# Kernel tuning notes

Measured on AMD Instinct MI355X. Metric: run time of the kernel, lower is better.

## Reference

```python
import jax, jax.numpy as jnp
import numpy as np
import math

B, T, D, H, FF = 2, 2048, 1024, 16, 4096
DH = D // H
EPS = 1e-5

def _ternary(key, out_f, in_f):
    # TFLELayer: ternary-quantized linear weight in {-1,0,1} (stored as f32 here)
    return jax.random.randint(key, (out_f, in_f), -1, 2).astype(jnp.float32)

def setup_inputs() -> dict:
    key = jax.random.key(0)
    ks = jax.random.split(key, 8)
    x = jax.random.normal(ks[0], (B, T, D), dtype=jnp.float32)
    mask = jnp.triu(jnp.ones((T, T), dtype=bool), k=1)  # True = masked (causal)
    return {
        "x": x,
        "mask": mask,
        "ln1_g": jnp.ones((D,), jnp.float32), "ln1_b": jnp.zeros((D,), jnp.float32),
        "ln2_g": jnp.ones((D,), jnp.float32), "ln2_b": jnp.zeros((D,), jnp.float32),
        "Wq": _ternary(ks[1], D, D), "Wk": _ternary(ks[2], D, D),
        "Wv": _ternary(ks[3], D, D), "Wo": _ternary(ks[4], D, D),
        "Wff1": _ternary(ks[5], FF, D), "Wff2": _ternary(ks[6], D, FF),
    }

def _ln(x, g, b):
    mu = jnp.mean(x, axis=-1, keepdims=True)
    var = jnp.var(x, axis=-1, keepdims=True)
    return (x - mu) * jax.lax.rsqrt(var + EPS) * g + b

def reference(x, mask, ln1_g, ln1_b, ln2_g, ln2_b, Wq, Wk, Wv, Wo, Wff1, Wff2):
    h = _ln(x, ln1_g, ln1_b)
    q = (h @ Wq.T).reshape(B, T, H, DH).transpose(0, 2, 1, 3)  # (B,H,T,DH)
    k = (h @ Wk.T).reshape(B, T, H, DH).transpose(0, 2, 1, 3)
    v = (h @ Wv.T).reshape(B, T, H, DH).transpose(0, 2, 1, 3)
    scale = 1.0 / math.sqrt(DH)
    attn = jnp.einsum('bhqd,bhkd->bhqk', q, k) * scale
    attn = jnp.where(mask[None, None], -jnp.inf, attn)
    attn = jax.nn.softmax(attn, axis=-1)
    out = jnp.einsum('bhqk,bhkd->bhqd', attn, v)
    out = out.transpose(0, 2, 1, 3).reshape(B, T, D) @ Wo.T
    x = x + out
    h = _ln(x, ln2_g, ln2_b)
    ff = jax.nn.gelu(h @ Wff1.T, approximate=False)
    ff = ff @ Wff2.T
    return x + ff
```

## Files before the change

### kernel.cpp

```cpp
#include <hip/hip_runtime.h>

typedef __bf16 bf16;
typedef bf16 bf16x8 __attribute__((ext_vector_type(8)));
typedef bf16 bf16x4 __attribute__((ext_vector_type(4)));
typedef float f32x4 __attribute__((ext_vector_type(4)));

static __device__ __forceinline__ void async16(const void* g, void* l) {
  __builtin_amdgcn_global_load_lds((__attribute__((address_space(1))) void*)g,
                                   (__attribute__((address_space(3))) void*)l,
                                   16, 0, 0);
}

template <int N>
static __device__ __forceinline__ float ror16(float x) {
  const int y =
      __builtin_amdgcn_update_dpp(0, __float_as_int(x), 0x120 | N, 0xf, 0xf, true);
  return __int_as_float(y);
}
static __device__ __forceinline__ float rowmax16(float x) {
  x = fmaxf(x, ror16<8>(x));
  x = fmaxf(x, ror16<4>(x));
  x = fmaxf(x, ror16<2>(x));
  x = fmaxf(x, ror16<1>(x));
  return x;
}
static __device__ __forceinline__ float rowsum16(float x) {
  x += ror16<8>(x);
  x += ror16<4>(x);
  x += ror16<2>(x);
  x += ror16<1>(x);
  return x;
}

__global__ __launch_bounds__(256) void ln1_cvt4(
    const float* __restrict__ x, const float* __restrict__ g,
    const float* __restrict__ b, bf16* __restrict__ hi, bf16* __restrict__ lo,
    const float* __restrict__ Wq, const float* __restrict__ Wk,
    const float* __restrict__ Wv, const float* __restrict__ Wo,
    bf16* __restrict__ wdst) {
  const int tid = threadIdx.x;
  if (blockIdx.x >= 4096) {
    const size_t i = ((size_t)(blockIdx.x - 4096) * 256 + tid) * 4;
    const size_t M1 = 1u << 20;
    const float* src = (i < M1) ? Wq : (i < 2 * M1) ? Wk : (i < 3 * M1) ? Wv : Wo;
    const size_t off = i & (M1 - 1);
    const float4 v = *(const float4*)(src + off);
    bf16x4 o = {(bf16)v.x, (bf16)v.y, (bf16)v.z, (bf16)v.w};
    *(bf16x4*)(wdst + i) = o;
    return;
  }
  const int row = blockIdx.x;
  const float* xr = x + (size_t)row * 1024;
  float v[4];
  float s1 = 0.f, s2 = 0.f;
#pragma unroll
  for (int j = 0; j < 4; ++j) {
    v[j] = xr[j * 256 + tid];
    s1 += v[j];
    s2 += v[j] * v[j];
  }
#pragma unroll
  for (int off = 1; off < 64; off <<= 1) {
    s1 += __shfl_xor(s1, off);
    s2 += __shfl_xor(s2, off);
  }
  __shared__ float ws1[4], ws2[4];
  const int wid = tid >> 6;
  if ((tid & 63) == 0) {
    ws1[wid] = s1;
    ws2[wid] = s2;
  }
  __syncthreads();
  s1 = ws1[0] + ws1[1] + ws1[2] + ws1[3];
  s2 = ws2[0] + ws2[1] + ws2[2] + ws2[3];
  const float mu = s1 * (1.f / 1024.f);
  const float var = s2 * (1.f / 1024.f) - mu * mu;
  const float rstd = 1.0f / sqrtf(var + 1e-5f);
#pragma unroll
  for (int j = 0; j < 4; ++j) {
    const int cc = j * 256 + tid;
    const float y = (v[j] - mu) * rstd * g[cc] + b[cc];
    const bf16 yh = (bf16)y;
    hi[(size_t)row * 1024 + cc] = yh;
    lo[(size_t)row * 1024 + cc] = (bf16)(y - (float)yh);
  }
}

__global__ __launch_bounds__(256) void ln_kernel(
    const float* __restrict__ x, const float* __restrict__ g,
    const float* __restrict__ b, bf16* __restrict__ hi) {
  const int row = blockIdx.x;
  const int tid = threadIdx.x;
  const float* xr = x + (size_t)row * 1024;
  float v[4];
  float s1 = 0.f, s2 = 0.f;
#pragma unroll
  for (int j = 0; j < 4; ++j) {
    v[j] = xr[j * 256 + tid];
    s1 += v[j];
    s2 += v[j] * v[j];
  }
#pragma unroll
  for (int off = 1; off < 64; off <<= 1) {
    s1 += __shfl_xor(s1, off);
    s2 += __shfl_xor(s2, off);
  }
  __shared__ float ws1[4], ws2[4];
  const int wid = tid >> 6;
  if ((tid & 63) == 0) {
    ws1[wid] = s1;
    ws2[wid] = s2;
  }
  __syncthreads();
  s1 = ws1[0] + ws1[1] + ws1[2] + ws1[3];
  s2 = ws2[0] + ws2[1] + ws2[2] + ws2[3];
  const float mu = s1 * (1.f / 1024.f);
  const float var = s2 * (1.f / 1024.f) - mu * mu;
  const float rstd = 1.0f / sqrtf(var + 1e-5f);
#pragma unroll
  for (int j = 0; j < 4; ++j) {
    const int cc = j * 256 + tid;
    const float y = (v[j] - mu) * rstd * g[cc] + b[cc];
    hi[(size_t)row * 1024 + cc] = (bf16)y;
  }
}

template <int EPI, bool SPLIT>
static __device__ __forceinline__ void gemm_body(
    const bf16* __restrict__ A, const bf16* __restrict__ A2,
    const bf16* __restrict__ B, void* __restrict__ Cv,
    const float* __restrict__ R, bf16* smem, int col0, int row0, int M, int N,
    int K) {
  bf16* sA = smem;
  bf16* sB = smem + 4096;
  const int tid = threadIdx.x;
  const int lane = tid & 63;
  const int wid = tid >> 6;
  const int wm = wid >> 1, wn = wid & 1;

  f32x4 acc[4][4];
  const f32x4 fzero = {0.f, 0.f, 0.f, 0.f};
#pragma unroll
  for (int i = 0; i < 4; ++i)
#pragma unroll
    for (int j = 0; j < 4; ++j) acc[i][j] = fzero;

  const int nk = K >> 5;
  const int total = SPLIT ? (nk << 1) : nk;
  const int r0 = tid >> 2, c0 = (tid & 3) << 3;
  const int r1 = (256 + tid) >> 2, c1 = ((256 + tid) & 3) << 3;
  bf16* lA0 = sA + (wid << 6) * 8;
  bf16* lA1 = sA + (256 + (wid << 6)) * 8;
  bf16* lB0 = sB + (wid << 6) * 8;
  bf16* lB1 = sB + (256 + (wid << 6)) * 8;

  for (int kt = 0; kt < total; ++kt) {
    const int kk = (kt < nk) ? kt : kt - nk;
    const bf16* Ap = (SPLIT && kt >= nk) ? A2 : A;
    const int k0 = kk << 5;
    async16(Ap + (size_t)(row0 + r0) * K + k0 + c0, lA0);
    async16(Ap + (size_t)(row0 + r1) * K + k0 + c1, lA1);
    async16(B + (size_t)(col0 + r0) * K + k0 + c0, lB0);
    async16(B + (size_t)(col0 + r1) * K + k0 + c1, lB1);
    __syncthreads();
    const int fr = lane & 15, fq = (lane >> 4) << 3;
    bf16x8 af[4], bfr[4];
#pragma unroll
    for (int i = 0; i < 4; ++i)
      af[i] = *(const bf16x8*)&sA[(wm * 64 + i * 16 + fr) * 32 + fq];
#pragma unroll
    for (int j = 0; j < 4; ++j)
      bfr[j] = *(const bf16x8*)&sB[(wn * 64 + j * 16 + fr) * 32 + fq];
#pragma unroll
    for (int i = 0; i < 4; ++i)
#pragma unroll
      for (int j = 0; j < 4; ++j)
        acc[i][j] = __builtin_amdgcn_mfma_f32_16x16x32_bf16(af[i], bfr[j],
                                                            acc[i][j], 0, 0, 0);
    __syncthreads();
  }

  const int fr = lane & 15, fq4 = (lane >> 4) << 2;
#pragma unroll
  for (int i = 0; i < 4; ++i) {
#pragma unroll
    for (int j = 0; j < 4; ++j) {
      const int rbase = row0 + wm * 64 + i * 16 + fq4;
      const int col = col0 + wn * 64 + j * 16 + fr;
      if constexpr (EPI == 5) {
        const int b = rbase >> 11, t = rbase & 2047;
        const int hh = col >> 6, d = col & 63;
        bf16x4 o4 = {(bf16)acc[i][j][0], (bf16)acc[i][j][1],
                     (bf16)acc[i][j][2], (bf16)acc[i][j][3]};
        *(bf16x4*)&((bf16*)Cv)[(((size_t)(b * 16 + hh)) * 64 + d) * 2048 + t] =
            o4;
      } else {
#pragma unroll
        for (int r = 0; r < 4; ++r) {
          const size_t idx = (size_t)(rbase + r) * N + col;
          const float val = acc[i][j][r];
          if constexpr (EPI == 0) {
            ((float*)Cv)[idx] = val;
          } else if constexpr (EPI == 2) {
            ((float*)Cv)[idx] = val + R[idx];
          } else {
            ((bf16*)Cv)[idx] =
                (bf16)(0.5f * val * (1.0f + erff(val * 0.7071067811865476f)));
          }
        }
      }
    }
  }
}

template <int EPI, bool SPLIT>
__global__ __launch_bounds__(256) void gemm_bt(
    const bf16* __restrict__ A, const bf16* __restrict__ A2,
    const bf16* __restrict__ B, void* __restrict__ Cv,
    const float* __restrict__ R, int M, int N, int K) {
  __shared__ bf16 smem[8192];
  gemm_body<EPI, SPLIT>(A, A2, B, Cv, R, smem, blockIdx.x * 128,
                        blockIdx.y * 128, M, N, K);
}

static __device__ __forceinline__ void gemm_split_merged(
    const bf16* __restrict__ A, const bf16* __restrict__ A2,
    const bf16* __restrict__ B, bf16* __restrict__ Chi, bf16* __restrict__ Clo,
    bf16* smem, float scale, int col0, int row0) {
  constexpr int K = 1024, N = 1024;
  bf16* sAh = smem;
  bf16* sAl = smem + 4096;
  bf16* sB = smem + 8192;
  const int tid = threadIdx.x;
  const int lane = tid & 63;
  const int wid = tid >> 6;
  const int wm = wid >> 1, wn = wid & 1;

  f32x4 acc[4][4];
  const f32x4 fzero = {0.f, 0.f, 0.f, 0.f};
#pragma unroll
  for (int i = 0; i < 4; ++i)
#pragma unroll
    for (int j = 0; j < 4; ++j) acc[i][j] = fzero;

  const int r0 = tid >> 2, c0 = (tid & 3) << 3;
  const int r1 = (256 + tid) >> 2, c1 = ((256 + tid) & 3) << 3;
  bf16* lAh0 = sAh + (wid << 6) * 8;
  bf16* lAh1 = sAh + (256 + (wid << 6)) * 8;
  bf16* lAl0 = sAl + (wid << 6) * 8;
  bf16* lAl1 = sAl + (256 + (wid << 6)) * 8;
  bf16* lB0 = sB + (wid << 6) * 8;
  bf16* lB1 = sB + (256 + (wid << 6)) * 8;

  for (int kt = 0; kt < 32; ++kt) {
    const int k0 = kt << 5;
    async16(A + (size_t)(row0 + r0) * K + k0 + c0, lAh0);
    async16(A + (size_t)(row0 + r1) * K + k0 + c1, lAh1);
    async16(A2 + (size_t)(row0 + r0) * K + k0 + c0, lAl0);
    async16(A2 + (size_t)(row0 + r1) * K + k0 + c1, lAl1);
    async16(B + (size_t)(col0 + r0) * K + k0 + c0, lB0);
    async16(B + (size_t)(col0 + r1) * K + k0 + c1, lB1);
    __syncthreads();
    const int fr = lane & 15, fq = (lane >> 4) << 3;
    bf16x8 ah[4], al[4], bfr[4];
#pragma unroll
    for (int i = 0; i < 4; ++i) {
      ah[i] = *(const bf16x8*)&sAh[(wm * 64 + i * 16 + fr) * 32 + fq];
      al[i] = *(const bf16x8*)&sAl[(wm * 64 + i * 16 + fr) * 32 + fq];
    }
#pragma unroll
    for (int j = 0; j < 4; ++j)
      bfr[j] = *(const bf16x8*)&sB[(wn * 64 + j * 16 + fr) * 32 + fq];
#pragma unroll
    for (int i = 0; i < 4; ++i)
#pragma unroll
      for (int j = 0; j < 4; ++j) {
        acc[i][j] = __builtin_amdgcn_mfma_f32_16x16x32_bf16(ah[i], bfr[j],
                                                            acc[i][j], 0, 0, 0);
        acc[i][j] = __builtin_amdgcn_mfma_f32_16x16x32_bf16(al[i], bfr[j],
                                                            acc[i][j], 0, 0, 0);
      }
    __syncthreads();
  }

  const int fr = lane & 15, fq4 = (lane >> 4) << 2;
#pragma unroll
  for (int i = 0; i < 4; ++i)
#pragma unroll
    for (int j = 0; j < 4; ++j) {
      const int rbase = row0 + wm * 64 + i * 16 + fq4;
      const int col = col0 + wn * 64 + j * 16 + fr;
#pragma unroll
      for (int r = 0; r < 4; ++r) {
        const size_t idx = (size_t)(rbase + r) * N + col;
        const float vs = acc[i][j][r] * scale;
        const bf16 hi = (bf16)vs;
        Chi[idx] = hi;
        Clo[idx] = (bf16)(vs - (float)hi);
      }
    }
}

__global__ __launch_bounds__(256) void gemm_qkv(
    const bf16* __restrict__ A, const bf16* __restrict__ A2,
    const bf16* __restrict__ Bq, const bf16* __restrict__ Bk,
    const bf16* __restrict__ Bv, bf16* qh, bf16* ql, bf16* kh, bf16* kl,
    bf16* vt) {
  __shared__ bf16 smem[12288];
  const int which = blockIdx.x >> 3;
  const int col0 = (blockIdx.x & 7) * 128, row0 = blockIdx.y * 128;
  if (which == 2) {
    gemm_body<5, false>(A, nullptr, Bv, (void*)vt, nullptr, smem, col0, row0,
                        4096, 1024, 1024);
  } else {
    gemm_split_merged(A, A2, which ? Bk : Bq, which ? kh : qh, which ? kl : ql,
                      smem, which ? 1.0f : 0.125f, col0, row0);
  }
}

template <int EPI>
__global__ __launch_bounds__(256) void gemm_bt64(
    const bf16* __restrict__ A, const bf16* __restrict__ B,
    void* __restrict__ Cv, const float* __restrict__ R, int M, int N, int K) {
  __shared__ bf16 sA[128 * 32];
  __shared__ bf16 sB[64 * 32];
  const int col0 = blockIdx.x * 64, row0 = blockIdx.y * 128;
  const int tid = threadIdx.x;
  const int lane = tid & 63;
  const int wid = tid >> 6;
  const int wm = wid >> 1, wn = wid & 1;

  f32x4 acc[4][2];
  const f32x4 fzero = {0.f, 0.f, 0.f, 0.f};
#pragma unroll
  for (int i = 0; i < 4; ++i)
#pragma unroll
    for (int j = 0; j < 2; ++j) acc[i][j] = fzero;

  const int nk = K >> 5;
  const int r0 = tid >> 2, c0 = (tid & 3) << 3;
  const int r1 = (256 + tid) >> 2, c1 = ((256 + tid) & 3) << 3;
  bf16* lA0 = sA + (wid << 6) * 8;
  bf16* lA1 = sA + (256 + (wid << 6)) * 8;
  bf16* lB0 = sB + (wid << 6) * 8;

  for (int kt = 0; kt < nk; ++kt) {
    const int k0 = kt << 5;
    async16(A + (size_t)(row0 + r0) * K + k0 + c0, lA0);
    async16(A + (size_t)(row0 + r1) * K + k0 + c1, lA1);
    async16(B + (size_t)(col0 + r0) * K + k0 + c0, lB0);
    __syncthreads();
    const int fr = lane & 15, fq = (lane >> 4) << 3;
    bf16x8 af[4], bfr[2];
#pragma unroll
    for (int i = 0; i < 4; ++i)
      af[i] = *(const bf16x8*)&sA[(wm * 64 + i * 16 + fr) * 32 + fq];
#pragma unroll
    for (int j = 0; j < 2; ++j)
      bfr[j] = *(const bf16x8*)&sB[(wn * 32 + j * 16 + fr) * 32 + fq];
#pragma unroll
    for (int i = 0; i < 4; ++i)
#pragma unroll
      for (int j = 0; j < 2; ++j)
        acc[i][j] = __builtin_amdgcn_mfma_f32_16x16x32_bf16(af[i], bfr[j],
                                                            acc[i][j], 0, 0, 0);
    __syncthreads();
  }

  const int fr = lane & 15, fq4 = (lane >> 4) << 2;
#pragma unroll
  for (int i = 0; i < 4; ++i) {
#pragma unroll
    for (int j = 0; j < 2; ++j) {
      const int rbase = row0 + wm * 64 + i * 16 + fq4;
      const int col = col0 + wn * 32 + j * 16 + fr;
#pragma unroll
      for (int r = 0; r < 4; ++r) {
        const size_t idx = (size_t)(rbase + r) * N + col;
        const float val = acc[i][j][r];
        if constexpr (EPI == 2) {
          ((float*)Cv)[idx] = val + R[idx];
        } else {
          ((float*)Cv)[idx] = val;
        }
      }
    }
  }
}

__global__ __launch_bounds__(256) void attn_cvt2(
    const bf16* __restrict__ qh_g, const bf16* __restrict__ ql_g,
    const bf16* __restrict__ kh_g, const bf16* __restrict__ kl_g,
    const bf16* __restrict__ vt_g, bf16* __restrict__ out,
    const float* __restrict__ Wf1, const float* __restrict__ Wf2,
    bf16* __restrict__ wdst) {
  __shared__ bf16 lds[18688];
  const int tid = threadIdx.x;
  if (blockIdx.x >= 1024) {
    const size_t i = ((size_t)(blockIdx.x - 1024) * 256 + tid) * 4;
    const size_t M4 = 4u << 20;
    const float* src = (i < M4) ? Wf1 : Wf2;
    const size_t off = (i < M4) ? i : i - M4;
    const float4 v = *(const float4*)(src + off);
    bf16x4 o4 = {(bf16)v.x, (bf16)v.y, (bf16)v.z, (bf16)v.w};
    *(bf16x4*)(wdst + i) = o4;
    return;
  }
  bf16* Kh = lds;
  bf16* Kl = lds + 4608;
  bf16* Vt = lds + 9216;
  bf16* Ps = lds + 13824;

  const int bid = blockIdx.x;
  const int qt = 31 - (bid >> 5);
  const int h = bid & 15;
  const int b = (bid >> 4) & 1;
  const int t0 = qt << 6;
  const int w = tid >> 6;
  const int lane = tid & 63;
  const int c = lane & 15;
  const int quad = lane >> 4;

  const int r0 = tid >> 3, c0 = (tid & 7) << 3;
  const int r1 = (tid + 256) >> 3, c1 = ((tid + 256) & 7) << 3;

  const size_t qrow =
      ((size_t)(b * 2048 + t0 + w * 16 + c)) * 1024 + h * 64 + quad * 8;
  bf16x8 aqh[2], aql[2];
  aqh[0] = *(const bf16x8*)&qh_g[qrow];
  aqh[1] = *(const bf16x8*)&qh_g[qrow + 32];
  aql[0] = *(const bf16x8*)&ql_g[qrow];
  aql[1] = *(const bf16x8*)&ql_g[qrow + 32];

  f32x4 o[4];
  const f32x4 fzero = {0.f, 0.f, 0.f, 0.f};
#pragma unroll
  for (int j = 0; j < 4; ++j) o[j] = fzero;
  float m_i[4] = {-3e38f, -3e38f, -3e38f, -3e38f};
  float l_i[4] = {0.f, 0.f, 0.f, 0.f};

  const size_t vtb = ((size_t)(b * 16 + h)) * 64 * 2048;
  const size_t kband = ((size_t)(b * 2048)) * 1024 + h * 64;

  bf16x8 gk[6];
  {
    gk[0] = *(const bf16x8*)&kh_g[kband + (size_t)r0 * 1024 + c0];
    gk[1] = *(const bf16x8*)&kh_g[kband + (size_t)r1 * 1024 + c1];
    gk[2] = *(const bf16x8*)&kl_g[kband + (size_t)r0 * 1024 + c0];
    gk[3] = *(const bf16x8*)&kl_g[kband + (size_t)r1 * 1024 + c1];
    gk[4] = *(const bf16x8*)&vt_g[vtb + (size_t)r0 * 2048 + c0];
    gk[5] = *(const bf16x8*)&vt_g[vtb + (size_t)r1 * 2048 + c1];
  }

  for (int kt = 0; kt <= qt; ++kt) {
    __syncthreads();
    *(bf16x8*)&Kh[r0 * 72 + c0] = gk[0];
    *(bf16x8*)&Kh[r1 * 72 + c1] = gk[1];
    *(bf16x8*)&Kl[r0 * 72 + c0] = gk[2];
    *(bf16x8*)&Kl[r1 * 72 + c1] = gk[3];
    *(bf16x8*)&Vt[r0 * 72 + c0] = gk[4];
    *(bf16x8*)&Vt[r1 * 72 + c1] = gk[5];
    __syncthreads();

    if (kt < qt) {
      const int kb1 = (kt + 1) << 6;
      const size_t kbase = kband + (size_t)kb1 * 1024;
      gk[0] = *(const bf16x8*)&kh_g[kbase + (size_t)r0 * 1024 + c0];
      gk[1] = *(const bf16x8*)&kh_g[kbase + (size_t)r1 * 1024 + c1];
      gk[2] = *(const bf16x8*)&kl_g[kbase + (size_t)r0 * 1024 + c0];
      gk[3] = *(const bf16x8*)&kl_g[kbase + (size_t)r1 * 1024 + c1];
      gk[4] = *(const bf16x8*)&vt_g[vtb + (size_t)r0 * 2048 + kb1 + c0];
      gk[5] = *(const bf16x8*)&vt_g[vtb + (size_t)r1 * 2048 + kb1 + c1];
    }

    bf16x8 bkh[4][2], bkl[4][2];
#pragma unroll
    for (int j = 0; j < 4; ++j)
#pragma unroll
      for (int s = 0; s < 2; ++s) {
        bkh[j][s] = *(const bf16x8*)&Kh[(j * 16 + c) * 72 + s * 32 + quad * 8];
        bkl[j][s] = *(const bf16x8*)&Kl[(j * 16 + c) * 72 + s * 32 + quad * 8];
      }

    f32x4 s4[4];
#pragma unroll
    for (int j = 0; j < 4; ++j) s4[j] = fzero;
#pragma unroll
    for (int j = 0; j < 4; ++j)
#pragma unroll
      for (int s = 0; s < 2; ++s) {
        s4[j] = __builtin_amdgcn_mfma_f32_16x16x32_bf16(aqh[s], bkh[j][s], s4[j], 0, 0, 0);
        s4[j] = __builtin_amdgcn_mfma_f32_16x16x32_bf16(aqh[s], bkl[j][s], s4[j], 0, 0, 0);
        s4[j] = __builtin_amdgcn_mfma_f32_16x16x32_bf16(aql[s], bkh[j][s], s4[j], 0, 0, 0);
      }

    if (kt == qt) {
#pragma unroll
      for (int j = 0; j < 4; ++j)
#pragma unroll
        for (int r = 0; r < 4; ++r)
          if (j * 16 + c > w * 16 + quad * 4 + r) s4[j][r] = -3e38f;
    }

    float al[4], p[4][4];
#pragma unroll
    for (int r = 0; r < 4; ++r) {
      float mt = fmaxf(fmaxf(s4[0][r], s4[1][r]), fmaxf(s4[2][r], s4[3][r]));
      mt = rowmax16(mt);
      const float mn = fmaxf(m_i[r], mt);
      al[r] = __expf(m_i[r] - mn);
      float ps = 0.f;
#pragma unroll
      for (int j = 0; j < 4; ++j) {
        p[r][j] = __expf(s4[j][r] - mn);
        ps += p[r][j];
      }
      ps = rowsum16(ps);
      l_i[r] = l_i[r] * al[r] + ps;
      m_i[r] = mn;
#pragma unroll
      for (int j = 0; j < 4; ++j) o[j][r] *= al[r];
    }

    bf16* Pw = Ps + w * 16 * 76;
#pragma unroll
    for (int r = 0; r < 4; ++r)
#pragma unroll
      for (int j = 0; j < 4; ++j)
        Pw[(quad * 4 + r) * 76 + j * 16 + c] = (bf16)p[r][j];

    bf16x8 ap[2], bv[4][2];
#pragma unroll
    for (int s = 0; s < 2; ++s)
      ap[s] = *(const bf16x8*)&Pw[c * 76 + s * 32 + quad * 8];
#pragma unroll
    for (int j = 0; j < 4; ++j)
#pragma unroll
      for (int s = 0; s < 2; ++s)
        bv[j][s] = *(const bf16x8*)&Vt[(j * 16 + c) * 72 + s * 32 + quad * 8];
#pragma unroll
    for (int j = 0; j < 4; ++j)
#pragma unroll
      for (int s = 0; s < 2; ++s)
        o[j] = __builtin_amdgcn_mfma_f32_16x16x32_bf16(ap[s], bv[j][s], o[j], 0, 0, 0);
  }

#pragma unroll
  for (int r = 0; r < 4; ++r) {
    const float inv = 1.0f / l_i[r];
#pragma unroll
    for (int j = 0; j < 4; ++j) {
      const size_t oi =
          ((size_t)(b * 2048 + t0 + w * 16 + quad * 4 + r)) * 1024 + h * 64 +
          j * 16 + c;
      out[oi] = (bf16)(o[j][r] * inv);
    }
  }
}

extern "C" void kernel_launch(void* const* d_in, const int* in_sizes, int n_in,
                              void* d_out, int out_size, void* d_ws,
                              size_t ws_size, hipStream_t stream) {
  const float* x = (const float*)d_in[0];
  const float* g1 = (const float*)d_in[2];
  const float* b1 = (const float*)d_in[3];
  const float* g2 = (const float*)d_in[4];
  const float* b2 = (const float*)d_in[5];
  const float* Wq = (const float*)d_in[6];
  const float* Wk = (const float*)d_in[7];
  const float* Wv = (const float*)d_in[8];
  const float* Wo = (const float*)d_in[9];
  const float* Wf1 = (const float*)d_in[10];
  const float* Wf2 = (const float*)d_in[11];
  char* ws = (char*)d_ws;
  const size_t MB = 1024 * 1024;
  const size_t M1 = 1u << 20;
  bf16* Wq_b = (bf16*)ws;
  bf16* Wk_b = Wq_b + 1 * M1;
  bf16* Wv_b = Wq_b + 2 * M1;
  bf16* Wo_b = Wq_b + 3 * M1;
  bf16* h_hi = (bf16*)(ws + 8 * MB);
  bf16* h_lo = (bf16*)(ws + 16 * MB);
  bf16* Wf1_b = h_hi;
  bf16* Wf2_b = h_lo;
  bf16* qh = (bf16*)(ws + 24 * MB);
  bf16* ql = (bf16*)(ws + 32 * MB);
  bf16* kh = (bf16*)(ws + 40 * MB);
  bf16* kl = (bf16*)(ws + 48 * MB);
  bf16* vt = (bf16*)(ws + 56 * MB);
  bf16* attnout = (bf16*)(ws + 64 * MB);
  float* x1 = (float*)qh;
  bf16* h2 = (bf16*)(ws + 72 * MB);
  bf16* ff = kh;
  float* outp = (float*)d_out;

  ln1_cvt4<<<8192, 256, 0, stream>>>(x, g1, b1, h_hi, h_lo, Wq, Wk, Wv, Wo,
                                     Wq_b);
  gemm_qkv<<<dim3(24, 32), 256, 0, stream>>>(h_hi, h_lo, Wq_b, Wk_b, Wv_b, qh,
                                             ql, kh, kl, vt);
  attn_cvt2<<<9216, 256, 0, stream>>>(qh, ql, kh, kl, vt, attnout, Wf1, Wf2,
                                      Wf1_b);
  gemm_bt64<2><<<dim3(16, 32), 256, 0, stream>>>(attnout, Wo_b, (void*)x1, x,
                                                 4096, 1024, 1024);
  ln_kernel<<<4096, 256, 0, stream>>>(x1, g2, b2, h2);
  gemm_bt<3, false><<<dim3(32, 32), 256, 0, stream>>>(
      h2, nullptr, Wf1_b, (void*)ff, nullptr, 4096, 4096, 1024);
  gemm_bt64<2><<<dim3(16, 32), 256, 0, stream>>>(ff, Wf2_b, (void*)outp, x1,
                                                 4096, 1024, 4096);
}
```

Baseline: 456.3 us.

## Double K-step per barrier in GEMMs and use exp2 with log2e-folded Q scale

All GEMM kernels now stage 64 K-elements per iteration, as two 32-wide LDS sub-tiles, which halves the number of __syncthreads pairs and loop iterations while doubling shared memory per block. Separately, the Q projection scale now folds in log2(e), so the attention softmax can use exp2f in place of __expf. The larger LDS footprint may reduce occupancy, and the unused SPLIT template path is removed.

```diff
diff --git a/kernel.cpp b/kernel.cpp
--- a/kernel.cpp
+++ b/kernel.cpp
@@ -125,14 +125,15 @@
   }
 }
 
-template <int EPI, bool SPLIT>
+template <int EPI>
 static __device__ __forceinline__ void gemm_body(
-    const bf16* __restrict__ A, const bf16* __restrict__ A2,
-    const bf16* __restrict__ B, void* __restrict__ Cv,
-    const float* __restrict__ R, bf16* smem, int col0, int row0, int M, int N,
-    int K) {
-  bf16* sA = smem;
-  bf16* sB = smem + 4096;
+    const bf16* __restrict__ A, const bf16* __restrict__ B,
+    void* __restrict__ Cv, const float* __restrict__ R, bf16* smem, int col0,
+    int row0, int M, int N, int K) {
+  bf16* sA0 = smem;
+  bf16* sA1 = smem + 4096;
+  bf16* sB0 = smem + 8192;
+  bf16* sB1 = smem + 12288;
   const int tid = threadIdx.x;
   const int lane = tid & 63;
   const int wid = tid >> 6;
@@ -145,38 +146,42 @@
 #pragma unroll
     for (int j = 0; j < 4; ++j) acc[i][j] = fzero;
 
-  const int nk = K >> 5;
-  const int total = SPLIT ? (nk << 1) : nk;
+  const int nk = K >> 6;
   const int r0 = tid >> 2, c0 = (tid & 3) << 3;
   const int r1 = (256 + tid) >> 2, c1 = ((256 + tid) & 3) << 3;
-  bf16* lA0 = sA + (wid << 6) * 8;
-  bf16* lA1 = sA + (256 + (wid << 6)) * 8;
-  bf16* lB0 = sB + (wid << 6) * 8;
-  bf16* lB1 = sB + (256 + (wid << 6)) * 8;
-
-  for (int kt = 0; kt < total; ++kt) {
-    const int kk = (kt < nk) ? kt : kt - nk;
-    const bf16* Ap = (SPLIT && kt >= nk) ? A2 : A;
-    const int k0 = kk << 5;
-    async16(Ap + (size_t)(row0 + r0) * K + k0 + c0, lA0);
-    async16(Ap + (size_t)(row0 + r1) * K + k0 + c1, lA1);
-    async16(B + (size_t)(col0 + r0) * K + k0 + c0, lB0);
-    async16(B + (size_t)(col0 + r1) * K + k0 + c1, lB1);
+  const int wofs0 = (wid << 6) * 8;
+  const int wofs1 = (256 + (wid << 6)) * 8;
+
+  for (int kt = 0; kt < nk; ++kt) {
+    const int k0 = kt << 6;
+    async16(A + (size_t)(row0 + r0) * K + k0 + c0, sA0 + wofs0);
+    async16(A + (size_t)(row0 + r1) * K + k0 + c1, sA0 + wofs1);
+    async16(A + (size_t)(row0 + r0) * K + k0 + 32 + c0, sA1 + wofs0);
+    async16(A + (size_t)(row0 + r1) * K + k0 + 32 + c1, sA1 + wofs1);
+    async16(B + (size_t)(col0 + r0) * K + k0 + c0, sB0 + wofs0);
+    async16(B + (size_t)(col0 + r1) * K + k0 + c1, sB0 + wofs1);
+    async16(B + (size_t)(col0 + r0) * K + k0 + 32 + c0, sB1 + wofs0);
+    async16(B + (size_t)(col0 + r1) * K + k0 + 32 + c1, sB1 + wofs1);
     __syncthreads();
     const int fr = lane & 15, fq = (lane >> 4) << 3;
-    bf16x8 af[4], bfr[4];
-#pragma unroll
-    for (int i = 0; i < 4; ++i)
-      af[i] = *(const bf16x8*)&sA[(wm * 64 + i * 16 + fr) * 32 + fq];
-#pragma unroll
-    for (int j = 0; j < 4; ++j)
-      bfr[j] = *(const bf16x8*)&sB[(wn * 64 + j * 16 + fr) * 32 + fq];
-#pragma unroll
-    for (int i = 0; i < 4; ++i)
+#pragma unroll
+    for (int t = 0; t < 2; ++t) {
+      const bf16* sA = t ? sA1 : sA0;
+      const bf16* sB = t ? sB1 : sB0;
+      bf16x8 af[4], bfr[4];
+#pragma unroll
+      for (int i = 0; i < 4; ++i)
+        af[i] = *(const bf16x8*)&sA[(wm * 64 + i * 16 + fr) * 32 + fq];
 #pragma unroll
       for (int j = 0; j < 4; ++j)
-        acc[i][j] = __builtin_amdgcn_mfma_f32_16x16x32_bf16(af[i], bfr[j],
-                                                            acc[i][j], 0, 0, 0);
+        bfr[j] = *(const bf16x8*)&sB[(wn * 64 + j * 16 + fr) * 32 + fq];
+#pragma unroll
+      for (int i = 0; i < 4; ++i)
+#pragma unroll
+        for (int j = 0; j < 4; ++j)
+          acc[i][j] = __builtin_amdgcn_mfma_f32_16x16x32_bf16(
+              af[i], bfr[j], acc[i][j], 0, 0, 0);
+    }
     __syncthreads();
   }
 
@@ -213,14 +218,13 @@
   }
 }
 
-template <int EPI, bool SPLIT>
+template <int EPI>
 __global__ __launch_bounds__(256) void gemm_bt(
-    const bf16* __restrict__ A, const bf16* __restrict__ A2,
-    const bf16* __restrict__ B, void* __restrict__ Cv,
-    const float* __restrict__ R, int M, int N, int K) {
-  __shared__ bf16 smem[8192];
-  gemm_body<EPI, SPLIT>(A, A2, B, Cv, R, smem, blockIdx.x * 128,
-                        blockIdx.y * 128, M, N, K);
+    const bf16* __restrict__ A, const bf16* __restrict__ B,
+    void* __restrict__ Cv, const float* __restrict__ R, int M, int N, int K) {
+  __shared__ bf16 smem[16384];
+  gemm_body<EPI>(A, B, Cv, R, smem, blockIdx.x * 128, blockIdx.y * 128, M, N,
+                 K);
 }
 
 static __device__ __forceinline__ void gemm_split_merged(
@@ -228,9 +232,12 @@
     const bf16* __restrict__ B, bf16* __restrict__ Chi, bf16* __restrict__ Clo,
     bf16* smem, float scale, int col0, int row0) {
   constexpr int K = 1024, N = 1024;
-  bf16* sAh = smem;
-  bf16* sAl = smem + 4096;
-  bf16* sB = smem + 8192;
+  bf16* sAh0 = smem;
+  bf16* sAh1 = smem + 4096;
+  bf16* sAl0 = smem + 8192;
+  bf16* sAl1 = smem + 12288;
+  bf16* sB0 = smem + 16384;
+  bf16* sB1 = smem + 20480;
   const int tid = threadIdx.x;
   const int lane = tid & 63;
   const int wid = tid >> 6;
@@ -245,41 +252,49 @@
 
   const int r0 = tid >> 2, c0 = (tid & 3) << 3;
   const int r1 = (256 + tid) >> 2, c1 = ((256 + tid) & 3) << 3;
-  bf16* lAh0 = sAh + (wid << 6) * 8;
-  bf16* lAh1 = sAh + (256 + (wid << 6)) * 8;
-  bf16* lAl0 = sAl + (wid << 6) * 8;
-  bf16* lAl1 = sAl + (256 + (wid << 6)) * 8;
-  bf16* lB0 = sB + (wid << 6) * 8;
-  bf16* lB1 = sB + (256 + (wid << 6)) * 8;
-
-  for (int kt = 0; kt < 32; ++kt) {
-    const int k0 = kt << 5;
-    async16(A + (size_t)(row0 + r0) * K + k0 + c0, lAh0);
-    async16(A + (size_t)(row0 + r1) * K + k0 + c1, lAh1);
-    async16(A2 + (size_t)(row0 + r0) * K + k0 + c0, lAl0);
-    async16(A2 + (size_t)(row0 + r1) * K + k0 + c1, lAl1);
-    async16(B + (size_t)(col0 + r0) * K + k0 + c0, lB0);
-    async16(B + (size_t)(col0 + r1) * K + k0 + c1, lB1);
+  const int wofs0 = (wid << 6) * 8;
+  const int wofs1 = (256 + (wid << 6)) * 8;
+
+  for (int kt = 0; kt < 16; ++kt) {
+    const int k0 = kt << 6;
+    async16(A + (size_t)(row0 + r0) * K + k0 + c0, sAh0 + wofs0);
+    async16(A + (size_t)(row0 + r1) * K + k0 + c1, sAh0 + wofs1);
+    async16(A + (size_t)(row0 + r0) * K + k0 + 32 + c0, sAh1 + wofs0);
+    async16(A + (size_t)(row0 + r1) * K + k0 + 32 + c1, sAh1 + wofs1);
+    async16(A2 + (size_t)(row0 + r0) * K + k0 + c0, sAl0 + wofs0);
+    async16(A2 + (size_t)(row0 + r1) * K + k0 + c1, sAl0 + wofs1);
+    async16(A2 + (size_t)(row0 + r0) * K + k0 + 32 + c0, sAl1 + wofs0);
+    async16(A2 + (size_t)(row0 + r1) * K + k0 + 32 + c1, sAl1 + wofs1);
+    async16(B + (size_t)(col0 + r0) * K + k0 + c0, sB0 + wofs0);
+    async16(B + (size_t)(col0 + r1) * K + k0 + c1, sB0 + wofs1);
+    async16(B + (size_t)(col0 + r0) * K + k0 + 32 + c0, sB1 + wofs0);
+    async16(B + (size_t)(col0 + r1) * K + k0 + 32 + c1, sB1 + wofs1);
     __syncthreads();
     const int fr = lane & 15, fq = (lane >> 4) << 3;
-    bf16x8 ah[4], al[4], bfr[4];
-#pragma unroll
-    for (int i = 0; i < 4; ++i) {
-      ah[i] = *(const bf16x8*)&sAh[(wm * 64 + i * 16 + fr) * 32 + fq];
-      al[i] = *(const bf16x8*)&sAl[(wm * 64 + i * 16 + fr) * 32 + fq];
-    }
-#pragma unroll
-    for (int j = 0; j < 4; ++j)
-      bfr[j] = *(const bf16x8*)&sB[(wn * 64 + j * 16 + fr) * 32 + fq];
-#pragma unroll
-    for (int i = 0; i < 4; ++i)
-#pragma unroll
-      for (int j = 0; j < 4; ++j) {
-        acc[i][j] = __builtin_amdgcn_mfma_f32_16x16x32_bf16(ah[i], bfr[j],
-                                                            acc[i][j], 0, 0, 0);
-        acc[i][j] = __builtin_amdgcn_mfma_f32_16x16x32_bf16(al[i], bfr[j],
-                                                            acc[i][j], 0, 0, 0);
+#pragma unroll
+    for (int t = 0; t < 2; ++t) {
+      const bf16* sAh = t ? sAh1 : sAh0;
+      const bf16* sAl = t ? sAl1 : sAl0;
+      const bf16* sB = t ? sB1 : sB0;
+      bf16x8 ah[4], al[4], bfr[4];
+#pragma unroll
+      for (int i = 0; i < 4; ++i) {
+        ah[i] = *(const bf16x8*)&sAh[(wm * 64 + i * 16 + fr) * 32 + fq];
+        al[i] = *(const bf16x8*)&sAl[(wm * 64 + i * 16 + fr) * 32 + fq];
       }
+#pragma unroll
+      for (int j = 0; j < 4; ++j)
+        bfr[j] = *(const bf16x8*)&sB[(wn * 64 + j * 16 + fr) * 32 + fq];
+#pragma unroll
+      for (int i = 0; i < 4; ++i)
+#pragma unroll
+        for (int j = 0; j < 4; ++j) {
+          acc[i][j] = __builtin_amdgcn_mfma_f32_16x16x32_bf16(
+              ah[i], bfr[j], acc[i][j], 0, 0, 0);
+          acc[i][j] = __builtin_amdgcn_mfma_f32_16x16x32_bf16(
+              al[i], bfr[j], acc[i][j], 0, 0, 0);
+        }
+    }
     __syncthreads();
   }
 
@@ -306,15 +321,16 @@
     const bf16* __restrict__ Bq, const bf16* __restrict__ Bk,
     const bf16* __restrict__ Bv, bf16* qh, bf16* ql, bf16* kh, bf16* kl,
     bf16* vt) {
-  __shared__ bf16 smem[12288];
+  __shared__ bf16 smem[24576];
   const int which = blockIdx.x >> 3;
   const int col0 = (blockIdx.x & 7) * 128, row0 = blockIdx.y * 128;
   if (which == 2) {
-    gemm_body<5, false>(A, nullptr, Bv, (void*)vt, nullptr, smem, col0, row0,
-                        4096, 1024, 1024);
+    gemm_body<5>(A, Bv, (void*)vt, nullptr, smem, col0, row0, 4096, 1024,
+                 1024);
   } else {
     gemm_split_merged(A, A2, which ? Bk : Bq, which ? kh : qh, which ? kl : ql,
-                      smem, which ? 1.0f : 0.125f, col0, row0);
+                      smem, which ? 1.0f : 0.125f * 1.44269504088896f, col0,
+                      row0);
   }
 }
 
@@ -322,8 +338,11 @@
 __global__ __launch_bounds__(256) void gemm_bt64(
     const bf16* __restrict__ A, const bf16* __restrict__ B,
     void* __restrict__ Cv, const float* __restrict__ R, int M, int N, int K) {
-  __shared__ bf16 sA[128 * 32];
-  __shared__ bf16 sB[64 * 32];
+  __shared__ bf16 smem[12288];
+  bf16* sA0 = smem;
+  bf16* sA1 = smem + 4096;
+  bf16* sB0 = smem + 8192;
+  bf16* sB1 = smem + 10240;
   const int col0 = blockIdx.x * 64, row0 = blockIdx.y * 128;
   const int tid = threadIdx.x;
   const int lane = tid & 63;
@@ -337,33 +356,40 @@
 #pragma unroll
     for (int j = 0; j < 2; ++j) acc[i][j] = fzero;
 
-  const int nk = K >> 5;
+  const int nk = K >> 6;
   const int r0 = tid >> 2, c0 = (tid & 3) << 3;
   const int r1 = (256 + tid) >> 2, c1 = ((256 + tid) & 3) << 3;
-  bf16* lA0 = sA + (wid << 6) * 8;
-  bf16* lA1 = sA + (256 + (wid << 6)) * 8;
-  bf16* lB0 = sB + (wid << 6) * 8;
+  const int wofs0 = (wid << 6) * 8;
+  const int wofs1 = (256 + (wid << 6)) * 8;
 
   for (int kt = 0; kt < nk; ++kt) {
-    const int k0 = kt << 5;
-    async16(A + (size_t)(row0 + r0) * K + k0 + c0, lA0);
-    async16(A + (size_t)(row0 + r1) * K + k0 + c1, lA1);
-    async16(B + (size_t)(col0 + r0) * K + k0 + c0, lB0);
+    const int k0 = kt << 6;
+    async16(A + (size_t)(row0 + r0) * K + k0 + c0, sA0 + wofs0);
+    async16(A + (size_t)(row0 + r1) * K + k0 + c1, sA0 + wofs1);
+    async16(A + (size_t)(row0 + r0) * K + k0 + 32 + c0, sA1 + wofs0);
+    async16(A + (size_t)(row0 + r1) * K + k0 + 32 + c1, sA1 + wofs1);
+    async16(B + (size_t)(col0 + r0) * K + k0 + c0, sB0 + wofs0);
+    async16(B + (size_t)(col0 + r0) * K + k0 + 32 + c0, sB1 + wofs0);
     __syncthreads();
     const int fr = lane & 15, fq = (lane >> 4) << 3;
-    bf16x8 af[4], bfr[2];
-#pragma unroll
-    for (int i = 0; i < 4; ++i)
-      af[i] = *(const bf16x8*)&sA[(wm * 64 + i * 16 + fr) * 32 + fq];
-#pragma unroll
-    for (int j = 0; j < 2; ++j)
-      bfr[j] = *(const bf16x8*)&sB[(wn * 32 + j * 16 + fr) * 32 + fq];
-#pragma unroll
-    for (int i = 0; i < 4; ++i)
+#pragma unroll
+    for (int t = 0; t < 2; ++t) {
+      const bf16* sA = t ? sA1 : sA0;
+      const bf16* sB = t ? sB1 : sB0;
+      bf16x8 af[4], bfr[2];
+#pragma unroll
+      for (int i = 0; i < 4; ++i)
+        af[i] = *(const bf16x8*)&sA[(wm * 64 + i * 16 + fr) * 32 + fq];
 #pragma unroll
       for (int j = 0; j < 2; ++j)
-        acc[i][j] = __builtin_amdgcn_mfma_f32_16x16x32_bf16(af[i], bfr[j],
-                                                            acc[i][j], 0, 0, 0);
+        bfr[j] = *(const bf16x8*)&sB[(wn * 32 + j * 16 + fr) * 32 + fq];
+#pragma unroll
+      for (int i = 0; i < 4; ++i)
+#pragma unroll
+        for (int j = 0; j < 2; ++j)
+          acc[i][j] = __builtin_amdgcn_mfma_f32_16x16x32_bf16(
+              af[i], bfr[j], acc[i][j], 0, 0, 0);
+    }
     __syncthreads();
   }
 
@@ -508,11 +534,11 @@
       float mt = fmaxf(fmaxf(s4[0][r], s4[1][r]), fmaxf(s4[2][r], s4[3][r]));
       mt = rowmax16(mt);
       const float mn = fmaxf(m_i[r], mt);
-      al[r] = __expf(m_i[r] - mn);
+      al[r] = exp2f(m_i[r] - mn);
       float ps = 0.f;
 #pragma unroll
       for (int j = 0; j < 4; ++j) {
-        p[r][j] = __expf(s4[j][r] - mn);
+        p[r][j] = exp2f(s4[j][r] - mn);
         ps += p[r][j];
       }
       ps = rowsum16(ps);
@@ -603,8 +629,8 @@
   gemm_bt64<2><<<dim3(16, 32), 256, 0, stream>>>(attnout, Wo_b, (void*)x1, x,
                                                  4096, 1024, 1024);
   ln_kernel<<<4096, 256, 0, stream>>>(x1, g2, b2, h2);
-  gemm_bt<3, false><<<dim3(32, 32), 256, 0, stream>>>(
-      h2, nullptr, Wf1_b, (void*)ff, nullptr, 4096, 4096, 1024);
+  gemm_bt<3><<<dim3(32, 32), 256, 0, stream>>>(h2, Wf1_b, (void*)ff, nullptr,
+                                               4096, 4096, 1024);
   gemm_bt64<2><<<dim3(16, 32), 256, 0, stream>>>(ff, Wf2_b, (void*)outp, x1,
                                                  4096, 1024, 4096);
 }
```

Result: faster. 418.7 us (-8.2%).
